# Kernel tuning notes

Measured on AMD Instinct MI355X. Metric: run time of the kernel, lower is better.

The kernel has to match this reference:

```python
import jax, jax.numpy as jnp
import numpy as np
import math

S, HID = 2048, 2048
NH, Q_LORA, KV_LORA = 16, 1536, 512
NOPE, ROPE, VDIM = 128, 64, 128
HEAD = NOPE + ROPE  # 192
BLK = 128
EPS = 1e-6
MSCALE = 0.1 * 1.0 * math.log(40.0) + 1.0
SOFTMAX_SCALE = HEAD ** -0.5 * MSCALE * MSCALE


def _dequant(w, s, blk=BLK):
    # w: [out,in] stored quantized values, s: [ceil(out/blk), ceil(in/blk)] block scale_inv
    so = jnp.repeat(s, blk, axis=0)[: w.shape[0]]
    se = jnp.repeat(so, blk, axis=1)[:, : w.shape[1]]
    return w * se


def _mm_dq(x, w, s):
    # mm_w8a16_dq_forward: x @ dequant(w).T
    return x @ _dequant(w, s).T


def _rmsnorm(x, w, eps=EPS):
    var = jnp.mean(x * x, axis=-1, keepdims=True)
    return x * jax.lax.rsqrt(var + eps) * w


def _rotate_half(x):
    h = x.shape[-1] // 2
    return jnp.concatenate([-x[..., h:], x[..., :h]], axis=-1)


def setup_inputs() -> dict:
    key = jax.random.key(0)
    ks = jax.random.split(key, 16)
    d = {
        'hidden_states': jax.random.normal(ks[0], (S, HID), jnp.float32),
        'wq_a': jax.random.normal(ks[1], (Q_LORA, HID), jnp.float32),
        'sq_a': jax.random.uniform(ks[2], (12, 16), jnp.float32) * 0.02 + 0.005,
        'wq_b': jax.random.normal(ks[3], (NH * HEAD, Q_LORA), jnp.float32),
        'sq_b': jax.random.uniform(ks[4], (24, 12), jnp.float32) * 0.02 + 0.005,
        'wkv_a': jax.random.normal(ks[5], (KV_LORA + ROPE, HID), jnp.float32),
        'skv_a': jax.random.uniform(ks[6], (5, 16), jnp.float32) * 0.02 + 0.005,
        'wkv_b': jax.random.normal(ks[7], (NH * (NOPE + VDIM), KV_LORA), jnp.float32),
        'skv_b': jax.random.uniform(ks[8], (32, 4), jnp.float32) * 0.02 + 0.005,
        'wo': jax.random.normal(ks[9], (HID, NH * VDIM), jnp.float32),
        'so': jax.random.uniform(ks[10], (16, 16), jnp.float32) * 0.02 + 0.005,
        'q_ln_w': jnp.ones((Q_LORA,), jnp.float32),
        'kv_ln_w': jnp.ones((KV_LORA,), jnp.float32),
    }
    pos = jnp.arange(S, dtype=jnp.float32)[:, None]
    inv = 1.0 / (10000.0 ** (jnp.arange(0, ROPE, 2, dtype=jnp.float32) / ROPE))
    ang = pos * inv[None, :]
    ang = jnp.concatenate([ang, ang], axis=-1)  # [S, 64]
    d['cos'] = jnp.cos(ang)
    d['sin'] = jnp.sin(ang)
    return d


def reference(hidden_states, cos, sin, wq_a, sq_a, wq_b, sq_b, wkv_a, skv_a,
              wkv_b, skv_b, wo, so, q_ln_w, kv_ln_w):
    # Q low-rank path: q_a -> rmsnorm -> q_b
    lq = _mm_dq(hidden_states, wq_a, sq_a)                 # [S, q_lora]
    q = _mm_dq(_rmsnorm(lq, q_ln_w), wq_b, sq_b)           # [S, NH*HEAD]
    q = q.reshape(S, NH, HEAD)
    q_nope, q_pe = q[..., :NOPE], q[..., NOPE:]            # [S,NH,128], [S,NH,64]

    # KV low-rank + MQA rope path
    lkv = _mm_dq(hidden_states, wkv_a, skv_a)              # [S, kv_lora+rope]
    kv_nope = _rmsnorm(lkv[:, :KV_LORA], kv_ln_w)          # [S, kv_lora]
    k_pe = lkv[:, KV_LORA:]                                # [S, 64] (shared across heads)
    kvb = _mm_dq(kv_nope, wkv_b, skv_b).reshape(S, NH, NOPE + VDIM)
    k_nope, v = kvb[..., :NOPE], kvb[..., NOPE:]           # [S,NH,128] each

    # RoPE (rotate-half) on the pe parts
    q_pe = q_pe * cos[:, None, :] + _rotate_half(q_pe) * sin[:, None, :]
    k_pe = k_pe * cos + _rotate_half(k_pe) * sin           # [S, 64]

    # prefill MLA attention with causal mask
    scores = (jnp.einsum('shd,thd->hst', q_nope, k_nope)
              + jnp.einsum('shd,td->hst', q_pe, k_pe)) * SOFTMAX_SCALE
    causal = jnp.tril(jnp.ones((S, S), bool))
    scores = jnp.where(causal[None], scores, -jnp.inf)
    probs = jax.nn.softmax(scores, axis=-1)                # [NH,S,S]
    attn = jnp.einsum('hst,thd->shd', probs, v).reshape(S, NH * VDIM)

    return _mm_dq(attn, wo, so)                            # [S, HID]
```

## Files before the change

kernel.cpp:

```cpp
#include <hip/hip_runtime.h>

typedef unsigned short u16;
typedef unsigned int u32;
typedef __attribute__((ext_vector_type(8))) short bf16x8;
typedef __attribute__((ext_vector_type(4))) float f32x4;
typedef __attribute__((ext_vector_type(16))) float f32x16;
typedef __attribute__((ext_vector_type(4))) unsigned short u16x4;

#define S_LEN 2048
#define HIDDEN 2048
#define NHEAD 16
#define QLORA 1536
#define KVLORA 512
#define NOPE_D 128
#define ROPE_D 64
#define V_D 128
#define HEAD_D 192
#define NCOMB 2176
#define LOG2E 1.442695041f

__device__ __constant__ float SM_SCALE_C = (float)(0.07216878364870323 *
    ((0.1 * 3.6888794541139363 + 1.0) * (0.1 * 3.6888794541139363 + 1.0)));

__device__ inline u16 f2bf(float f) {
    union { float f; unsigned int u; } v; v.f = f;
    unsigned int r = v.u + 0x7FFFu + ((v.u >> 16) & 1u);
    return (u16)(r >> 16);
}
__device__ inline float bf2f(u16 b) {
    union { unsigned int u; float f; } v; v.u = ((unsigned int)b) << 16;
    return v.f;
}
__device__ inline void gload_lds16(const u16* g, u16* l) {
    __builtin_amdgcn_global_load_lds(
        (const __attribute__((address_space(1))) void*)g,
        (__attribute__((address_space(3))) void*)l, 16, 0, 0);
}

__device__ __forceinline__ int xcd_swizzle(int orig, int nwg) {
    int qq = nwg >> 3, rr = nwg & 7, xcd = orig & 7, loc = orig >> 3;
    return (xcd < rr) ? (xcd * (qq + 1) + loc)
                      : (rr * (qq + 1) + (xcd - rr) * qq + loc);
}

__global__ __launch_bounds__(256)
void prep_weights(const float* __restrict__ hs,
                  const float* __restrict__ wq_a, const float* __restrict__ sq_a,
                  const float* __restrict__ wq_b, const float* __restrict__ sq_b,
                  const float* __restrict__ wkv_a, const float* __restrict__ skv_a,
                  const float* __restrict__ wkv_b, const float* __restrict__ skv_b,
                  const float* __restrict__ wo, const float* __restrict__ so,
                  u16* __restrict__ hs_bf, u16* __restrict__ wcomb,
                  u16* __restrict__ wqb_bf, u16* __restrict__ wkvb_bf,
                  u16* __restrict__ wo_bf) {
    int r = blockIdx.x * 4 + (threadIdx.x >> 6);
    const float* W; const float* Sc; u16* out; int n, K, sc_cols;
    if (r < 2048)       { W = hs;    Sc = 0;      out = hs_bf;   n = r;        K = 2048; sc_cols = 0; }
    else if (r < 3584)  { W = wq_a;  Sc = sq_a;   out = wcomb;   n = r - 2048; K = 2048; sc_cols = 16; }
    else if (r < 4160)  { W = wkv_a; Sc = skv_a;  out = wcomb + (size_t)QLORA * 2048; n = r - 3584; K = 2048; sc_cols = 16; }
    else if (r < 7232)  { W = wq_b;  Sc = sq_b;   out = wqb_bf;  n = r - 4160; K = 1536; sc_cols = 12; }
    else if (r < 11328) { W = wkv_b; Sc = skv_b;  out = wkvb_bf; n = r - 7232; K = 512;  sc_cols = 4; }
    else                { W = wo;    Sc = so;     out = wo_bf;   n = r - 11328; K = 2048; sc_cols = 16; }
    for (int k = (threadIdx.x & 63) * 8; k < K; k += 512) {
        float sc = Sc ? Sc[(n >> 7) * sc_cols + (k >> 7)] : 1.0f;
        f32x4 v0 = *(const f32x4*)(W + (size_t)n * K + k);
        f32x4 v1 = *(const f32x4*)(W + (size_t)n * K + k + 4);
        bf16x8 o;
        #pragma unroll
        for (int i = 0; i < 4; ++i) {
            o[i]     = (short)f2bf(v0[i] * sc);
            o[i + 4] = (short)f2bf(v1[i] * sc);
        }
        *(bf16x8*)(out + (size_t)n * K + k) = o;
    }
}

__device__ __forceinline__ void gemm_core(
    const u16* __restrict__ A, const u16* __restrict__ W, u16* __restrict__ C,
    int M, int N, int Ktot, int Ksub, int bm, int bn, int bz,
    u16 (*As)[128 * 64], u16 (*Ws)[128 * 64]) {
    const int tid = threadIdx.x;
    const int lane = tid & 63;
    const int wv = tid >> 6;
    const int wm = wv >> 1, wn = wv & 1;
    const int lr = lane & 15, lk = lane >> 4;
    const int srow = lane >> 3;
    const int schunk = lane & 7;

    f32x4 acc[4][4] = {};

    const int kbeg = bz * Ksub;
    const int nst = Ksub >> 6;

    auto stage = [&](int buf, int k0) {
        #pragma unroll
        for (int i = 0; i < 4; ++i) {
            int t = (wv * 4 + i) * 8 + srow;
            int cs = (schunk ^ (t & 7)) << 3;
            gload_lds16(A + (size_t)(bm + t) * Ktot + k0 + cs, &As[buf][(wv * 4 + i) * 512]);
            gload_lds16(W + (size_t)(bn + t) * Ktot + k0 + cs, &Ws[buf][(wv * 4 + i) * 512]);
        }
    };

    stage(0, kbeg);
    __syncthreads();
    int cur = 0;
    for (int t = 0; t < nst; ++t) {
        if (t + 1 < nst) stage(cur ^ 1, kbeg + (t + 1) * 64);
        #pragma unroll
        for (int kh = 0; kh < 2; ++kh) {
            bf16x8 af[4], bfr[4];
            #pragma unroll
            for (int mi = 0; mi < 4; ++mi) {
                int r = wm * 64 + mi * 16 + lr;
                af[mi] = *(const bf16x8*)&As[cur][r * 64 + (((kh * 4 + lk) ^ (lr & 7)) << 3)];
            }
            #pragma unroll
            for (int ni = 0; ni < 4; ++ni) {
                int r = wn * 64 + ni * 16 + lr;
                bfr[ni] = *(const bf16x8*)&Ws[cur][r * 64 + (((kh * 4 + lk) ^ (lr & 7)) << 3)];
            }
            __builtin_amdgcn_s_setprio(1);
            #pragma unroll
            for (int mi = 0; mi < 4; ++mi)
                #pragma unroll
                for (int ni = 0; ni < 4; ++ni)
                    acc[mi][ni] = __builtin_amdgcn_mfma_f32_16x16x32_bf16(af[mi], bfr[ni], acc[mi][ni], 0, 0, 0);
            __builtin_amdgcn_s_setprio(0);
        }
        __syncthreads();
        cur ^= 1;
    }

    u16* Pb = C + (size_t)bz * M * N;
    #pragma unroll
    for (int mi = 0; mi < 4; ++mi)
        #pragma unroll
        for (int ni = 0; ni < 4; ++ni)
            #pragma unroll
            for (int j = 0; j < 4; ++j) {
                int r = bm + wm * 64 + mi * 16 + lk * 4 + j;
                int c = bn + wn * 64 + ni * 16 + lr;
                if (c < N) Pb[(size_t)r * N + c] = f2bf(acc[mi][ni][j]);
            }
}

__global__ __launch_bounds__(256)
void gemm_bf16(const u16* __restrict__ A, const u16* __restrict__ W,
               u16* __restrict__ C, int M, int N, int Ktot, int Ksub) {
    __shared__ u16 As[2][128 * 64];
    __shared__ u16 Ws[2][128 * 64];
    const int gx = gridDim.x, gy = gridDim.y;
    const int nwg = gx * gy * gridDim.z;
    const int orig = blockIdx.x + gx * (blockIdx.y + gy * blockIdx.z);
    const int wg = xcd_swizzle(orig, nwg);
    const int bn = (wg % gx) * 128;
    const int bm = ((wg / gx) % gy) * 128;
    const int bz = wg / (gx * gy);
    gemm_core(A, W, C, M, N, Ktot, Ksub, bm, bn, bz, As, Ws);
}

__global__ __launch_bounds__(256)
void gemm_qh_kvb(const u16* __restrict__ lqn, const u16* __restrict__ wqb, u16* __restrict__ arena,
                 const u16* __restrict__ kvn, const u16* __restrict__ wkvb, u16* __restrict__ kvb) {
    __shared__ u16 As[2][128 * 64];
    __shared__ u16 Ws[2][128 * 64];
    const int NWG = 24 * 16 * 3 + 32 * 16;
    const int wg = xcd_swizzle(blockIdx.x, NWG);
    if (wg < 24 * 16 * 3) {
        const int bn = (wg % 24) * 128;
        const int bm = ((wg / 24) % 16) * 128;
        const int bz = wg / (24 * 16);
        gemm_core(lqn, wqb, arena, S_LEN, NHEAD * HEAD_D, QLORA, 512, bm, bn, bz, As, Ws);
    } else {
        const int w2 = wg - 24 * 16 * 3;
        const int bn = (w2 % 32) * 128;
        const int bm = (w2 / 32) * 128;
        gemm_core(kvn, wkvb, kvb, S_LEN, NHEAD * 256, KVLORA, 512, bm, bn, 0, As, Ws);
    }
}

__global__ __launch_bounds__(256)
void reduce_rms_comb(const u16* __restrict__ P,
                     const float* __restrict__ q_ln, const float* __restrict__ kv_ln,
                     u16* __restrict__ lqn, u16* __restrict__ kvn, u16* __restrict__ kpe) {
    __shared__ float vbuf[NCOMB];
    __shared__ float r2[2][4];
    const int row = blockIdx.x;
    const u16* p0 = P + (size_t)row * NCOMB;
    const size_t st = (size_t)S_LEN * NCOMB;
    float ssq = 0.f, ssk = 0.f;
    for (int c = threadIdx.x * 8; c < NCOMB; c += 2048) {
        bf16x8 a0 = *(const bf16x8*)(p0 + c);
        bf16x8 a1 = *(const bf16x8*)(p0 + st + c);
        bf16x8 a2 = *(const bf16x8*)(p0 + 2 * st + c);
        bf16x8 a3 = *(const bf16x8*)(p0 + 3 * st + c);
        float s = 0.f;
        #pragma unroll
        for (int j = 0; j < 8; ++j) {
            float v = bf2f((u16)a0[j]) + bf2f((u16)a1[j]) + bf2f((u16)a2[j]) + bf2f((u16)a3[j]);
            vbuf[c + j] = v;
            s += v * v;
        }
        if (c < QLORA) ssq += s;
        else if (c < QLORA + KVLORA) ssk += s;
    }
    #pragma unroll
    for (int off = 1; off < 64; off <<= 1) {
        ssq += __shfl_xor(ssq, off, 64);
        ssk += __shfl_xor(ssk, off, 64);
    }
    if ((threadIdx.x & 63) == 0) {
        r2[0][threadIdx.x >> 6] = ssq;
        r2[1][threadIdx.x >> 6] = ssk;
    }
    __syncthreads();
    float rsq = rsqrtf((r2[0][0] + r2[0][1] + r2[0][2] + r2[0][3]) / (float)QLORA + 1e-6f);
    float rsk = rsqrtf((r2[1][0] + r2[1][1] + r2[1][2] + r2[1][3]) / (float)KVLORA + 1e-6f);
    for (int c = threadIdx.x * 8; c < NCOMB; c += 2048) {
        bf16x8 o;
        if (c < QLORA) {
            #pragma unroll
            for (int j = 0; j < 8; ++j) o[j] = (short)f2bf(vbuf[c + j] * rsq * q_ln[c + j]);
            *(bf16x8*)(lqn + (size_t)row * QLORA + c) = o;
        } else if (c < QLORA + KVLORA) {
            int cc = c - QLORA;
            #pragma unroll
            for (int j = 0; j < 8; ++j) o[j] = (short)f2bf(vbuf[c + j] * rsk * kv_ln[cc + j]);
            *(bf16x8*)(kvn + (size_t)row * KVLORA + cc) = o;
        } else if (c < QLORA + KVLORA + ROPE_D) {
            int cc = c - QLORA - KVLORA;
            #pragma unroll
            for (int j = 0; j < 8; ++j) o[j] = (short)f2bf(vbuf[c + j]);
            *(bf16x8*)(kpe + (size_t)row * ROPE_D + cc) = o;
        }
    }
}

__global__ __launch_bounds__(256)
void prep_qkv_frag(const u16* __restrict__ P, const u16* __restrict__ kvb,
                   const u16* __restrict__ kpe, const float* __restrict__ cosb,
                   const float* __restrict__ sinb, u16* __restrict__ qfrag,
                   u16* __restrict__ kfrag, u16* __restrict__ vfrag) {
    __shared__ u16 Vs[32][136];
    const int sblk = blockIdx.x, h = blockIdx.y;
    if (blockIdx.z == 0) {
        const float sm = SM_SCALE_C;
        const size_t st = (size_t)S_LEN * (NHEAD * HEAD_D);
        #pragma unroll
        for (int c = 0; c < 3; ++c) {
            int idx = c * 256 + threadIdx.x;
            int kk = idx >> 6;
            int lane = idx & 63;
            int s = sblk * 32 + (lane & 31);
            int d0 = kk * 16 + (lane >> 5) * 8;
            const u16* p0 = P + (size_t)s * (NHEAD * HEAD_D) + h * HEAD_D;
            float x[8];
            {
                bf16x8 a0 = *(const bf16x8*)(p0 + d0);
                bf16x8 a1 = *(const bf16x8*)(p0 + st + d0);
                bf16x8 a2 = *(const bf16x8*)(p0 + 2 * st + d0);
                #pragma unroll
                for (int j = 0; j < 8; ++j)
                    x[j] = bf2f((u16)a0[j]) + bf2f((u16)a1[j]) + bf2f((u16)a2[j]);
            }
            bf16x8 o;
            if (d0 < NOPE_D) {
                #pragma unroll
                for (int j = 0; j < 8; ++j) o[j] = (short)f2bf(x[j] * sm);
            } else {
                int r0 = d0 - NOPE_D;
                int rp = (r0 + 32) & 63;
                float rv[8];
                bf16x8 b0 = *(const bf16x8*)(p0 + NOPE_D + rp);
                bf16x8 b1 = *(const bf16x8*)(p0 + st + NOPE_D + rp);
                bf16x8 b2 = *(const bf16x8*)(p0 + 2 * st + NOPE_D + rp);
                #pragma unroll
                for (int j = 0; j < 8; ++j)
                    rv[j] = bf2f((u16)b0[j]) + bf2f((u16)b1[j]) + bf2f((u16)b2[j]);
                float sign = (r0 < 32) ? -1.f : 1.f;
                #pragma unroll
                for (int j = 0; j < 8; ++j) {
                    float cs = cosb[s * ROPE_D + r0 + j];
                    float sn = sinb[s * ROPE_D + r0 + j];
                    o[j] = (short)f2bf((x[j] * cs + sign * rv[j] * sn) * sm);
                }
            }
            *(bf16x8*)(qfrag + (((size_t)h * 64 + sblk) * 12 + kk) * 512 + lane * 8) = o;
        }
    } else {
        #pragma unroll
        for (int it = 0; it < 2; ++it) {
            int idx = it * 256 + threadIdx.x;
            int r = idx >> 4;
            int c8 = (idx & 15) * 8;
            int s = sblk * 32 + r;
            *(bf16x8*)&Vs[r][c8] = *(const bf16x8*)(kvb + (size_t)s * (NHEAD * 256) + h * 256 + NOPE_D + c8);
        }
        #pragma unroll
        for (int c = 0; c < 3; ++c) {
            int idx = c * 256 + threadIdx.x;
            int kk = idx >> 6;
            int lane = idx & 63;
            int s = sblk * 32 + (lane & 31);
            int d0 = kk * 16 + (lane >> 5) * 8;
            bf16x8 o;
            if (d0 < NOPE_D) {
                o = *(const bf16x8*)(kvb + (size_t)s * (NHEAD * 256) + h * 256 + d0);
            } else {
                int r0 = d0 - NOPE_D;
                const u16* kp = kpe + (size_t)s * ROPE_D;
                bf16x8 x = *(const bf16x8*)(kp + r0);
                bf16x8 rv = *(const bf16x8*)(kp + ((r0 + 32) & 63));
                float sign = (r0 < 32) ? -1.f : 1.f;
                #pragma unroll
                for (int j = 0; j < 8; ++j) {
                    float cs = cosb[s * ROPE_D + r0 + j];
                    float sn = sinb[s * ROPE_D + r0 + j];
                    o[j] = (short)f2bf(bf2f((u16)x[j]) * cs + sign * bf2f((u16)rv[j]) * sn);
                }
            }
            *(bf16x8*)(kfrag + (((size_t)h * 64 + sblk) * 12 + kk) * 512 + lane * 8) = o;
        }
        __syncthreads();
        #pragma unroll
        for (int it = 0; it < 2; ++it) {
            int idx = it * 256 + threadIdx.x;
            int fi = idx >> 6;
            int lane = idx & 63;
            int bb = fi >> 1, h16 = fi & 1;
            int col = bb * 32 + (lane & 31);
            int row0 = h16 * 16 + (lane >> 5) * 8;
            bf16x8 o;
            #pragma unroll
            for (int j = 0; j < 8; ++j) o[j] = (short)Vs[row0 + j][col];
            *(bf16x8*)(vfrag + (((size_t)h * 64 + sblk) * 8 + fi) * 512 + lane * 8) = o;
        }
    }
}

__global__ void reduce_out(const u16* __restrict__ P, float* __restrict__ out, int n) {
    int i = (blockIdx.x * blockDim.x + threadIdx.x) * 8;
    if (i >= n) return;
    bf16x8 a0 = *(const bf16x8*)(P + i);
    bf16x8 a1 = *(const bf16x8*)(P + (size_t)n + i);
    bf16x8 a2 = *(const bf16x8*)(P + 2 * (size_t)n + i);
    bf16x8 a3 = *(const bf16x8*)(P + 3 * (size_t)n + i);
    f32x4 o0, o1;
    #pragma unroll
    for (int j = 0; j < 4; ++j) {
        o0[j] = bf2f((u16)a0[j]) + bf2f((u16)a1[j]) + bf2f((u16)a2[j]) + bf2f((u16)a3[j]);
        o1[j] = bf2f((u16)a0[j + 4]) + bf2f((u16)a1[j + 4]) + bf2f((u16)a2[j + 4]) + bf2f((u16)a3[j + 4]);
    }
    *(f32x4*)(out + i) = o0;
    *(f32x4*)(out + i + 4) = o1;
}

__global__ __launch_bounds__(256, 2)
void flash_attn4(const u16* __restrict__ qfrag, const u16* __restrict__ kfrag,
                 const u16* __restrict__ vfrag, u16* __restrict__ attn) {
    __shared__ float OB[3][128][32];
    __shared__ float MB[3][2][32];

    const int tid = threadIdx.x, lane = tid & 63, wq = tid >> 6;
    const int b = blockIdx.x;
    const int t = 63 - (b >> 4);
    const int h = ((b & 7) << 1) | ((b >> 3) & 1);
    const int q0 = t * 32;
    const int lq = lane & 31;
    const int hi = lane >> 5;

    const int n = t + 1;
    const int s_lo = (wq * n) >> 2;
    const int s_hi = ((wq + 1) * n) >> 2;

    bf16x8 qfr[12];
    {
        const u16* qb = qfrag + (((size_t)h * 64 + t) * 12) * 512 + lane * 8;
        #pragma unroll
        for (int kk = 0; kk < 12; ++kk) qfr[kk] = *(const bf16x8*)(qb + kk * 512);
    }

    const u16* kfb = kfrag + ((size_t)h * 64 * 12) * 512 + lane * 8;
    const u16* vfb = vfrag + ((size_t)h * 64 * 8) * 512 + lane * 8;

    f32x16 oa[4] = {};
    float mrun = -3.0e38f, lrun = 0.f;

    bf16x8 kcur[12];
    {
        int psub = (s_lo < s_hi) ? s_lo : 0;
        const u16* kp = kfb + (size_t)psub * 12 * 512;
        #pragma unroll
        for (int kk = 0; kk < 12; ++kk)
            kcur[kk] = *(const bf16x8*)(kp + kk * 512);
    }

    for (int sub = s_lo; sub < s_hi; ++sub) {
        f32x16 s0 = {}, s1 = {};
        __builtin_amdgcn_s_setprio(1);
        #pragma unroll
        for (int kk = 0; kk < 12; kk += 2) {
            s0 = __builtin_amdgcn_mfma_f32_32x32x16_bf16(kcur[kk], qfr[kk], s0, 0, 0, 0);
            s1 = __builtin_amdgcn_mfma_f32_32x32x16_bf16(kcur[kk + 1], qfr[kk + 1], s1, 0, 0, 0);
        }
        __builtin_amdgcn_s_setprio(0);
        {
            int nsub = (sub + 1 < s_hi) ? sub + 1 : sub;
            const u16* kp = kfb + (size_t)nsub * 12 * 512;
            #pragma unroll
            for (int kk = 0; kk < 12; ++kk)
                kcur[kk] = *(const bf16x8*)(kp + kk * 512);
        }
        bf16x8 va[8];
        {
            const u16* vp = vfb + (size_t)sub * 8 * 512;
            #pragma unroll
            for (int fi = 0; fi < 8; ++fi)
                va[fi] = *(const bf16x8*)(vp + fi * 512);
        }
        f32x16 sv = s0 + s1;
        if (sub == t) {
            #pragma unroll
            for (int r = 0; r < 16; ++r) {
                int krow = (r & 3) + 8 * (r >> 2) + 4 * hi;
                if (krow > lq) sv[r] = -3.0e38f;
            }
        }
        float tm = sv[0];
        #pragma unroll
        for (int r = 1; r < 16; ++r) tm = fmaxf(tm, sv[r]);
        tm = fmaxf(tm, __shfl_xor(tm, 32, 64));
        if (!__all(tm - mrun <= 8.f)) {
            float mn = fmaxf(mrun, tm);
            float scl = exp2f((mrun - mn) * LOG2E);
            mrun = mn;
            lrun *= scl;
            #pragma unroll
            for (int bb = 0; bb < 4; ++bb)
                #pragma unroll
                for (int r = 0; r < 16; ++r) oa[bb][r] *= scl;
        }
        float p[16];
        float psum = 0.f;
        #pragma unroll
        for (int r = 0; r < 16; ++r) {
            p[r] = exp2f((sv[r] - mrun) * LOG2E);
            psum += p[r];
        }
        psum += __shfl_xor(psum, 32, 64);
        lrun += psum;
        u32 pw[8], sw[8];
        #pragma unroll
        for (int i = 0; i < 8; ++i)
            pw[i] = (u32)f2bf(p[2 * i]) | ((u32)f2bf(p[2 * i + 1]) << 16);
        #pragma unroll
        for (int i = 0; i < 8; ++i)
            sw[i] = (u32)__shfl_xor((int)pw[i], 32, 64);
        union { u32 w[4]; bf16x8 v; } bf0, bf1;
        bf0.w[0] = hi ? sw[2] : pw[0];
        bf0.w[1] = hi ? sw[3] : pw[1];
        bf0.w[2] = hi ? pw[2] : sw[0];
        bf0.w[3] = hi ? pw[3] : sw[1];
        bf1.w[0] = hi ? sw[6] : pw[4];
        bf1.w[1] = hi ? sw[7] : pw[5];
        bf1.w[2] = hi ? pw[6] : sw[4];
        bf1.w[3] = hi ? pw[7] : sw[5];
        __builtin_amdgcn_s_setprio(1);
        #pragma unroll
        for (int bb = 0; bb < 4; ++bb) {
            oa[bb] = __builtin_amdgcn_mfma_f32_32x32x16_bf16(va[bb * 2],     bf0.v, oa[bb], 0, 0, 0);
            oa[bb] = __builtin_amdgcn_mfma_f32_32x32x16_bf16(va[bb * 2 + 1], bf1.v, oa[bb], 0, 0, 0);
        }
        __builtin_amdgcn_s_setprio(0);
    }

    if (wq) {
        #pragma unroll
        for (int bb = 0; bb < 4; ++bb)
            #pragma unroll
            for (int r = 0; r < 16; ++r) {
                int dv = bb * 32 + (r & 3) + 8 * (r >> 2) + 4 * hi;
                OB[wq - 1][dv][lq] = oa[bb][r];
            }
        if (lane < 32) {
            MB[wq - 1][0][lane] = mrun;
            MB[wq - 1][1][lane] = lrun;
        }
    }
    __syncthreads();
    if (!wq) {
        float m1 = MB[0][0][lq], l1 = MB[0][1][lq];
        float m2 = MB[1][0][lq], l2 = MB[1][1][lq];
        float m3 = MB[2][0][lq], l3 = MB[2][1][lq];
        float M = fmaxf(fmaxf(mrun, m1), fmaxf(m2, m3));
        float e0 = exp2f((mrun - M) * LOG2E);
        float e1 = exp2f((m1 - M) * LOG2E);
        float e2 = exp2f((m2 - M) * LOG2E);
        float e3 = exp2f((m3 - M) * LOG2E);
        float L = lrun * e0 + l1 * e1 + l2 * e2 + l3 * e3;
        float inv = 1.0f / L;
        u16* ob = attn + (size_t)(q0 + lq) * (NHEAD * V_D) + h * V_D;
        #pragma unroll
        for (int bb = 0; bb < 4; ++bb)
            #pragma unroll
            for (int rq = 0; rq < 4; ++rq) {
                u16x4 pk;
                #pragma unroll
                for (int rb = 0; rb < 4; ++rb) {
                    int r = rq * 4 + rb;
                    int dv = bb * 32 + rb + 8 * rq + 4 * hi;
                    float o = (oa[bb][r] * e0 + OB[0][dv][lq] * e1 +
                               OB[1][dv][lq] * e2 + OB[2][dv][lq] * e3) * inv;
                    pk[rb] = f2bf(o);
                }
                *(u16x4*)(ob + bb * 32 + 8 * rq + 4 * hi) = pk;
            }
    }
}

extern "C" void kernel_launch(void* const* d_in, const int* in_sizes, int n_in,
                              void* d_out, int out_size, void* d_ws, size_t ws_size,
                              hipStream_t stream) {
    const float* hs    = (const float*)d_in[0];
    const float* wq_a  = (const float*)d_in[1];
    const float* sq_a  = (const float*)d_in[2];
    const float* wq_b  = (const float*)d_in[3];
    const float* sq_b  = (const float*)d_in[4];
    const float* wkv_a = (const float*)d_in[5];
    const float* skv_a = (const float*)d_in[6];
    const float* wkv_b = (const float*)d_in[7];
    const float* skv_b = (const float*)d_in[8];
    const float* wo    = (const float*)d_in[9];
    const float* so    = (const float*)d_in[10];
    const float* q_ln  = (const float*)d_in[11];
    const float* kv_ln = (const float*)d_in[12];
    const float* cosb  = (const float*)d_in[13];
    const float* sinb  = (const float*)d_in[14];
    float* out = (float*)d_out;

    char* ws = (char*)d_ws;
    size_t off = 0;
    auto alloc = [&](size_t bytes) -> void* {
        void* p = ws + off; off += (bytes + 255) & ~(size_t)255; return p;
    };
    u16* hs_bf  = (u16*)alloc((size_t)S_LEN * HIDDEN * 2);
    u16* lqn    = (u16*)alloc((size_t)S_LEN * QLORA * 2);
    u16* kvn    = (u16*)alloc((size_t)S_LEN * KVLORA * 2);
    u16* kpe    = (u16*)alloc((size_t)S_LEN * ROPE_D * 2);
    u16* kvb    = (u16*)alloc((size_t)S_LEN * NHEAD * 256 * 2);
    u16* attn   = (u16*)alloc((size_t)S_LEN * NHEAD * V_D * 2);
    u16* qfrag  = (u16*)alloc((size_t)NHEAD * 64 * 12 * 512 * 2);
    u16* kfrag  = (u16*)alloc((size_t)NHEAD * 64 * 12 * 512 * 2);
    u16* vfrag  = (u16*)alloc((size_t)NHEAD * 64 * 8 * 512 * 2);
    u16* wcomb  = (u16*)alloc((size_t)NCOMB * HIDDEN * 2);
    u16* wqb_bf  = (u16*)alloc((size_t)(NHEAD * HEAD_D) * QLORA * 2);
    u16* wkvb_bf = (u16*)alloc((size_t)(NHEAD * 256) * KVLORA * 2);
    u16* wo_bf   = (u16*)alloc((size_t)HIDDEN * (NHEAD * V_D) * 2);
    u16* arena  = (u16*)alloc((size_t)3 * S_LEN * (NHEAD * HEAD_D) * 2);

    prep_weights<<<3344, 256, 0, stream>>>(
        hs, wq_a, sq_a, wq_b, sq_b, wkv_a, skv_a, wkv_b, skv_b, wo, so,
        hs_bf, wcomb, wqb_bf, wkvb_bf, wo_bf);

    gemm_bf16<<<dim3(NCOMB / 128, S_LEN / 128, 4), 256, 0, stream>>>(hs_bf, wcomb, arena,
        S_LEN, NCOMB, HIDDEN, HIDDEN / 4);
    reduce_rms_comb<<<S_LEN, 256, 0, stream>>>(arena, q_ln, kv_ln, lqn, kvn, kpe);

    gemm_qh_kvb<<<24 * 16 * 3 + 32 * 16, 256, 0, stream>>>(lqn, wqb_bf, arena, kvn, wkvb_bf, kvb);

    prep_qkv_frag<<<dim3(64, NHEAD, 2), 256, 0, stream>>>(arena, kvb, kpe, cosb, sinb,
        qfrag, kfrag, vfrag);

    flash_attn4<<<1024, 256, 0, stream>>>(qfrag, kfrag, vfrag, attn);

    gemm_bf16<<<dim3(16, 16, 4), 256, 0, stream>>>(attn, wo_bf, arena,
        S_LEN, HIDDEN, NHEAD * V_D, (NHEAD * V_D) / 4);
    reduce_out<<<S_LEN * HIDDEN / 8 / 256, 256, 0, stream>>>(arena, out, S_LEN * HIDDEN);
}
```

Measured before the change: 199.0 us.

## Prefetch V fragments one step ahead and use packed bf16 conversion intrinsics

The V fragment loads in the attention loop move to a software prefetch. The next step's V is loaded after the PV MFMAs, mirroring the existing K prefetch, so global load latency overlaps the softmax and score computation. The manual bf16 rounding is also replaced with HIP's __float22bfloat162_rn packed conversion, which may map to a hardware pack-convert instruction, in both the weight cast kernel and the probability packing. The prefetch holds 8 more bf16x8 registers live across the loop, which raises register pressure and may cost occupancy.

```diff
diff --git a/kernel.cpp b/kernel.cpp
--- a/kernel.cpp
+++ b/kernel.cpp
@@ -1,4 +1,5 @@
 #include <hip/hip_runtime.h>
+#include <hip/hip_bf16.h>
 
 typedef unsigned short u16;
 typedef unsigned int u32;
@@ -23,9 +24,13 @@
     ((0.1 * 3.6888794541139363 + 1.0) * (0.1 * 3.6888794541139363 + 1.0)));
 
 __device__ inline u16 f2bf(float f) {
-    union { float f; unsigned int u; } v; v.f = f;
-    unsigned int r = v.u + 0x7FFFu + ((v.u >> 16) & 1u);
-    return (u16)(r >> 16);
+    __hip_bfloat16 h = __float2bfloat16(f);
+    return *reinterpret_cast<u16*>(&h);
+}
+__device__ inline u32 pack2bf(float lo, float hi) {
+    float2 v = make_float2(lo, hi);
+    __hip_bfloat162 h2 = __float22bfloat162_rn(v);
+    return *reinterpret_cast<u32*>(&h2);
 }
 __device__ inline float bf2f(u16 b) {
     union { unsigned int u; float f; } v; v.u = ((unsigned int)b) << 16;
@@ -65,13 +70,13 @@
         float sc = Sc ? Sc[(n >> 7) * sc_cols + (k >> 7)] : 1.0f;
         f32x4 v0 = *(const f32x4*)(W + (size_t)n * K + k);
         f32x4 v1 = *(const f32x4*)(W + (size_t)n * K + k + 4);
-        bf16x8 o;
-        #pragma unroll
-        for (int i = 0; i < 4; ++i) {
-            o[i]     = (short)f2bf(v0[i] * sc);
-            o[i + 4] = (short)f2bf(v1[i] * sc);
-        }
-        *(bf16x8*)(out + (size_t)n * K + k) = o;
+        u32 w[4];
+        w[0] = pack2bf(v0[0] * sc, v0[1] * sc);
+        w[1] = pack2bf(v0[2] * sc, v0[3] * sc);
+        w[2] = pack2bf(v1[0] * sc, v1[1] * sc);
+        w[3] = pack2bf(v1[2] * sc, v1[3] * sc);
+        *(__attribute__((ext_vector_type(4))) u32*)(out + (size_t)n * K + k) =
+            *( __attribute__((ext_vector_type(4))) u32*)w;
     }
 }
 
@@ -387,13 +392,17 @@
     f32x16 oa[4] = {};
     float mrun = -3.0e38f, lrun = 0.f;
 
-    bf16x8 kcur[12];
+    bf16x8 kcur[12], vcur[8];
     {
         int psub = (s_lo < s_hi) ? s_lo : 0;
         const u16* kp = kfb + (size_t)psub * 12 * 512;
         #pragma unroll
         for (int kk = 0; kk < 12; ++kk)
             kcur[kk] = *(const bf16x8*)(kp + kk * 512);
+        const u16* vp = vfb + (size_t)psub * 8 * 512;
+        #pragma unroll
+        for (int fi = 0; fi < 8; ++fi)
+            vcur[fi] = *(const bf16x8*)(vp + fi * 512);
     }
 
     for (int sub = s_lo; sub < s_hi; ++sub) {
@@ -411,13 +420,6 @@
             #pragma unroll
             for (int kk = 0; kk < 12; ++kk)
                 kcur[kk] = *(const bf16x8*)(kp + kk * 512);
-        }
-        bf16x8 va[8];
-        {
-            const u16* vp = vfb + (size_t)sub * 8 * 512;
-            #pragma unroll
-            for (int fi = 0; fi < 8; ++fi)
-                va[fi] = *(const bf16x8*)(vp + fi * 512);
         }
         f32x16 sv = s0 + s1;
         if (sub == t) {
@@ -453,7 +455,7 @@
         u32 pw[8], sw[8];
         #pragma unroll
         for (int i = 0; i < 8; ++i)
-            pw[i] = (u32)f2bf(p[2 * i]) | ((u32)f2bf(p[2 * i + 1]) << 16);
+            pw[i] = pack2bf(p[2 * i], p[2 * i + 1]);
         #pragma unroll
         for (int i = 0; i < 8; ++i)
             sw[i] = (u32)__shfl_xor((int)pw[i], 32, 64);
@@ -469,10 +471,17 @@
         __builtin_amdgcn_s_setprio(1);
         #pragma unroll
         for (int bb = 0; bb < 4; ++bb) {
-            oa[bb] = __builtin_amdgcn_mfma_f32_32x32x16_bf16(va[bb * 2],     bf0.v, oa[bb], 0, 0, 0);
-            oa[bb] = __builtin_amdgcn_mfma_f32_32x32x16_bf16(va[bb * 2 + 1], bf1.v, oa[bb], 0, 0, 0);
+            oa[bb] = __builtin_amdgcn_mfma_f32_32x32x16_bf16(vcur[bb * 2],     bf0.v, oa[bb], 0, 0, 0);
+            oa[bb] = __builtin_amdgcn_mfma_f32_32x32x16_bf16(vcur[bb * 2 + 1], bf1.v, oa[bb], 0, 0, 0);
         }
         __builtin_amdgcn_s_setprio(0);
+        {
+            int nsub = (sub + 1 < s_hi) ? sub + 1 : sub;
+            const u16* vp = vfb + (size_t)nsub * 8 * 512;
+            #pragma unroll
+            for (int fi = 0; fi < 8; ++fi)
+                vcur[fi] = *(const bf16x8*)(vp + fi * 512);
+        }
     }
 
     if (wq) {
```

Measured after the change: 197.4 us. No clear change (-0.8%).
